# Optimization experiments

Measured on AMD Instinct MI355X. Metric: run time of the kernel, lower is better.

The kernel has to match this reference:

```python
import jax, jax.numpy as jnp
import numpy as np

N_LEVELS = 16
N_FEATS = 2
TABLE_SIZE = 1 << 19          # log2_hashmap_size = 19
BASE_RES = 32
PER_LEVEL_SCALE = 1.3819
RES = 512
CLAMP = 25.133
PRIME_Y = np.uint32(2654435761)
N_PTS = 1 << 19


def hashgrid_encode(table, uv):
    """Instant-NGP style multires hashgrid. table: [L, T, F], uv: [N, 2] in [0,1].
    Returns [N, L*F]."""
    L, T, F = table.shape
    levels = jnp.arange(L)
    res = jnp.floor(BASE_RES * (PER_LEVEL_SCALE ** levels.astype(jnp.float32))).astype(jnp.int32)  # [L]
    # 4 bilinear corner offsets
    offs = jnp.array([[0, 0], [1, 0], [0, 1], [1, 1]], dtype=jnp.int32)  # [4, 2]

    def level_fn(tab_l, res_l):
        pos = uv * res_l.astype(uv.dtype)                       # [N, 2]
        p0 = jnp.clip(jnp.floor(pos).astype(jnp.int32), 0, res_l - 1)
        frac = pos - p0.astype(uv.dtype)                        # [N, 2]
        corners = p0[:, None, :] + offs[None, :, :]             # [N, 4, 2]
        cx = corners[..., 0].astype(jnp.uint32)
        cy = corners[..., 1].astype(jnp.uint32)
        stride = (res_l + 1).astype(jnp.uint32)
        dense_idx = cx + cy * stride                            # dense grid index
        hash_idx = (cx ^ (cy * PRIME_Y)) & jnp.uint32(T - 1)    # spatial hash (T is pow2)
        use_dense = (res_l + 1).astype(jnp.int64) * (res_l + 1).astype(jnp.int64) <= T
        idx = jnp.where(use_dense, dense_idx, hash_idx).astype(jnp.int32)  # [N, 4]
        feats = tab_l[idx]                                      # [N, 4, F] gather
        wx, wy = frac[:, 0], frac[:, 1]
        w = jnp.stack([(1 - wx) * (1 - wy), wx * (1 - wy),
                       (1 - wx) * wy, wx * wy], axis=-1)        # [N, 4]
        return jnp.einsum('ncf,nc->nf', feats, w)               # [N, F]

    out = jax.vmap(level_fn)(table, res)                        # [L, N, F]
    return out.transpose(1, 0, 2).reshape(uv.shape[0], L * F)


def sin_layer(x, W, b):
    h = jnp.clip(x @ W.T + b, -CLAMP, CLAMP)
    return jnp.sin(h)


def setup_inputs() -> dict:
    key = jax.random.key(0)
    ks = jax.random.split(key, 8)
    y = jax.random.randint(ks[0], (N_PTS,), 0, RES, dtype=jnp.int32)
    x = jax.random.randint(ks[1], (N_PTS,), 0, RES, dtype=jnp.int32)
    cam_feat = jax.random.normal(ks[2], (32,), dtype=jnp.float32)
    # NGP tables initialized uniform in [-1e-4, 1e-4]
    table = jax.random.uniform(ks[3], (N_LEVELS, TABLE_SIZE, N_FEATS),
                               minval=-1e-4, maxval=1e-4, dtype=jnp.float32)
    def siren_w(k, outp, inp):
        return jax.random.uniform(k, (outp, inp), minval=-1.0 / inp, maxval=1.0 / inp,
                                  dtype=jnp.float32)
    W1 = siren_w(ks[4], 512, 64)
    W2 = siren_w(ks[5], 512, 512)
    W3 = siren_w(ks[6], 384, 512)
    return {"y": y, "x": x, "cam_feat": cam_feat, "table": table,
            "W1": W1, "b1": jnp.zeros((512,), jnp.float32),
            "W2": W2, "b2": jnp.zeros((512,), jnp.float32),
            "W3": W3, "b3": jnp.zeros((384,), jnp.float32)}


def reference(y, x, cam_feat, table, W1, b1, W2, b2, W3, b3):
    denom = jnp.float32(RES - 1)
    uv = jnp.stack([jnp.clip(x.astype(jnp.float32), 0, RES - 1) / denom,
                    jnp.clip(y.astype(jnp.float32), 0, RES - 1) / denom], axis=-1)  # [N, 2]
    codes = hashgrid_encode(table, uv)                          # [N, 32]
    cam = jnp.broadcast_to(cam_feat[None, :], (codes.shape[0], cam_feat.shape[0]))
    h = jnp.concatenate([codes, cam], axis=-1)                  # [N, 64]
    h = sin_layer(h, W1, b1)
    h = sin_layer(h, W2, b2)
    return sin_layer(h, W3, b3)                                 # [N, 384]
```

## Files before the change

### kernel.cpp

```cpp
#include <hip/hip_runtime.h>

typedef _Float16 half8 __attribute__((ext_vector_type(8)));
typedef _Float16 half4 __attribute__((ext_vector_type(4)));
typedef _Float16 half2v __attribute__((ext_vector_type(2)));
typedef float f32x4 __attribute__((ext_vector_type(4)));

#define TSIZE (1 << 19)
#define TMASK (TSIZE - 1)

__constant__ int c_res[16] = {32, 44, 61, 84, 116, 161, 222, 307,
                              425, 588, 812, 1123, 1551, 2144, 2963, 4095};

__global__ void hg_cvt_all(const float* __restrict__ W1, const float* __restrict__ W2,
                           const float* __restrict__ W3, _Float16* __restrict__ d) {
  int g = blockIdx.x * blockDim.x + threadIdx.x;
  int i = g * 4;
  const float* s;
  if (i < 32768) s = W1 + i;
  else if (i < 32768 + 262144) s = W2 + (i - 32768);
  else s = W3 + (i - 32768 - 262144);
  float4 v = *(const float4*)s;
  half4 h = {(_Float16)v.x, (_Float16)v.y, (_Float16)v.z, (_Float16)v.w};
  *(half4*)(d + i) = h;
}

__device__ __forceinline__ float sin_act(float x) {
  if (__builtin_expect(fabsf(x) > 1.0f, 0))
    return sinf(fminf(fmaxf(x, -25.133f), 25.133f));
  float x2 = x * x;
  float p = 2.75573192e-6f;
  p = fmaf(p, x2, -1.98412698e-4f);
  p = fmaf(p, x2, 8.33333333e-3f);
  p = fmaf(p, x2, -1.66666667e-1f);
  return fmaf(p * x2, x, x);
}

#define XROW 144
#define SBASE 9216
#define SROW 1040
#define LD_X(m, k) (*(const half8*)(&smem[(m) * XROW + (k) * 2]))
#define LD_S(m, k) (*(const half8*)(&smem[SBASE + (m) * SROW + (k) * 2]))
#define ST_S8(m, n, v) \
  do { *(half4*)(&smem[SBASE + (m) * SROW + (n) * 2]) = (v); } while (0)

#define MFMA16 __builtin_amdgcn_mfma_f32_16x16x32_f16

__global__ void __launch_bounds__(512, 4)
hg_fused(const int* __restrict__ ybuf, const int* __restrict__ xbuf,
         const float* __restrict__ cam, const float* __restrict__ table,
         const _Float16* __restrict__ W1h, const float* __restrict__ b1,
         const _Float16* __restrict__ W2h, const float* __restrict__ b2,
         const _Float16* __restrict__ W3h, const float* __restrict__ b3,
         float* __restrict__ out) {
  __shared__ __align__(16) unsigned char smem[75776];
  const int t = threadIdx.x;
  const int lane = t & 63;
  const int wid = t >> 6;
  const int l15 = lane & 15;
  const int lhi = lane >> 4;
  const int pbase = blockIdx.x << 6;
  const f32x4 vzero = {0.f, 0.f, 0.f, 0.f};

  {
    const int sub = t & 15;
    const int res = c_res[sub];
    const float rf = (float)res;
    const unsigned strd = (unsigned)(res + 1);
    const bool dense = (res <= 723);
    const float* tb = table + ((size_t)sub * TSIZE) * 2;
    const float2 cf = ((const float2*)cam)[sub];
    const half2v hc = {(_Float16)cf.x, (_Float16)cf.y};
#pragma unroll
    for (int hh = 0; hh < 2; ++hh) {
      const int m = (t >> 4) + hh * 32;
      const int p = pbase + m;
      const float u = (float)xbuf[p] / 511.0f;
      const float v = (float)ybuf[p] / 511.0f;
      const float px = u * rf, py = v * rf;
      int p0x = (int)floorf(px); p0x = p0x < 0 ? 0 : (p0x > res - 1 ? res - 1 : p0x);
      int p0y = (int)floorf(py); p0y = p0y < 0 ? 0 : (p0y > res - 1 ? res - 1 : p0y);
      const float fx = px - (float)p0x, fy = py - (float)p0y;
      const float w00 = (1.f - fx) * (1.f - fy), w10 = fx * (1.f - fy);
      const float w01 = (1.f - fx) * fy, w11 = fx * fy;
      float c0 = 0.f, c1 = 0.f;
#pragma unroll
      for (int c = 0; c < 4; ++c) {
        const unsigned cx = (unsigned)(p0x + (c & 1));
        const unsigned cy = (unsigned)(p0y + (c >> 1));
        const unsigned idx = dense ? (cx + cy * strd)
                                   : ((cx ^ (cy * 2654435761u)) & TMASK);
        const float2 f = *(const float2*)(tb + (size_t)idx * 2);
        const float w = (c == 0) ? w00 : (c == 1) ? w10 : (c == 2) ? w01 : w11;
        c0 = fmaf(w, f.x, c0);
        c1 = fmaf(w, f.y, c1);
      }
      half2v hf = {(_Float16)c0, (_Float16)c1};
      *(half2v*)(&smem[m * XROW + 4 * sub]) = hf;
      *(half2v*)(&smem[m * XROW + 64 + 4 * sub]) = hc;
    }
  }
  __syncthreads();

  {
    const int n0 = wid << 6;
    f32x4 acc[4][4];
#pragma unroll
    for (int i = 0; i < 4; ++i)
#pragma unroll
      for (int j = 0; j < 4; ++j) acc[i][j] = vzero;
#pragma unroll
    for (int ks = 0; ks < 2; ++ks) {
      const int kk = ks * 32 + lhi * 8;
      half8 bw[4];
#pragma unroll
      for (int nf = 0; nf < 4; ++nf)
        bw[nf] = *(const half8*)(W1h + (n0 + nf * 16 + l15) * 64 + kk);
      half8 ax[4];
#pragma unroll
      for (int mf = 0; mf < 4; ++mf) ax[mf] = LD_X(mf * 16 + l15, kk);
#pragma unroll
      for (int mf = 0; mf < 4; ++mf)
#pragma unroll
        for (int nf = 0; nf < 4; ++nf)
          acc[mf][nf] = MFMA16(bw[nf], ax[mf], acc[mf][nf], 0, 0, 0);
    }
#pragma unroll
    for (int nf = 0; nf < 4; ++nf) {
      const int nb = n0 + nf * 16 + lhi * 4;
      const f32x4 bb = *(const f32x4*)(b1 + nb);
#pragma unroll
      for (int mf = 0; mf < 4; ++mf) {
        half4 pk;
#pragma unroll
        for (int r = 0; r < 4; ++r) pk[r] = (_Float16)sin_act(acc[mf][nf][r] + bb[r]);
        ST_S8(mf * 16 + l15, nb, pk);
      }
    }
  }
  __syncthreads();

  {
    const int n0 = wid << 6;
    f32x4 acc[4][4];
#pragma unroll
    for (int i = 0; i < 4; ++i)
#pragma unroll
      for (int j = 0; j < 4; ++j) acc[i][j] = vzero;
#pragma unroll 4
    for (int ks = 0; ks < 16; ++ks) {
      const int kk = ks * 32 + lhi * 8;
      half8 bw[4];
#pragma unroll
      for (int nf = 0; nf < 4; ++nf)
        bw[nf] = *(const half8*)(W2h + (n0 + nf * 16 + l15) * 512 + kk);
      half8 ax[4];
#pragma unroll
      for (int mf = 0; mf < 4; ++mf) ax[mf] = LD_S(mf * 16 + l15, kk);
#pragma unroll
      for (int mf = 0; mf < 4; ++mf)
#pragma unroll
        for (int nf = 0; nf < 4; ++nf)
          acc[mf][nf] = MFMA16(bw[nf], ax[mf], acc[mf][nf], 0, 0, 0);
    }
    half4 pk[4][4];
#pragma unroll
    for (int nf = 0; nf < 4; ++nf) {
      const f32x4 bb = *(const f32x4*)(b2 + (n0 + nf * 16 + lhi * 4));
#pragma unroll
      for (int mf = 0; mf < 4; ++mf)
#pragma unroll
        for (int r = 0; r < 4; ++r)
          pk[nf][mf][r] = (_Float16)sin_act(acc[mf][nf][r] + bb[r]);
    }
    __syncthreads();
#pragma unroll
    for (int nf = 0; nf < 4; ++nf) {
      const int nb = n0 + nf * 16 + lhi * 4;
#pragma unroll
      for (int mf = 0; mf < 4; ++mf) ST_S8(mf * 16 + l15, nb, pk[nf][mf]);
    }
  }
  __syncthreads();

  {
    const int n0 = wid * 48;
    f32x4 acc[4][3];
#pragma unroll
    for (int i = 0; i < 4; ++i)
#pragma unroll
      for (int j = 0; j < 3; ++j) acc[i][j] = vzero;
#pragma unroll 4
    for (int ks = 0; ks < 16; ++ks) {
      const int kk = ks * 32 + lhi * 8;
      half8 bw[3];
#pragma unroll
      for (int nf = 0; nf < 3; ++nf)
        bw[nf] = *(const half8*)(W3h + (n0 + nf * 16 + l15) * 512 + kk);
      half8 ax[4];
#pragma unroll
      for (int mf = 0; mf < 4; ++mf) ax[mf] = LD_S(mf * 16 + l15, kk);
#pragma unroll
      for (int mf = 0; mf < 4; ++mf)
#pragma unroll
        for (int nf = 0; nf < 3; ++nf)
          acc[mf][nf] = MFMA16(bw[nf], ax[mf], acc[mf][nf], 0, 0, 0);
    }
#pragma unroll
    for (int nf = 0; nf < 3; ++nf) {
      const int nb = n0 + nf * 16 + lhi * 4;
      const f32x4 bb = *(const f32x4*)(b3 + nb);
#pragma unroll
      for (int mf = 0; mf < 4; ++mf) {
        float4 o;
        float* op = &o.x;
#pragma unroll
        for (int r = 0; r < 4; ++r) op[r] = sin_act(acc[mf][nf][r] + bb[r]);
        *(float4*)(out + (size_t)(pbase + mf * 16 + l15) * 384 + nb) = o;
      }
    }
  }
}

extern "C" void kernel_launch(void* const* d_in, const int* in_sizes, int n_in,
                              void* d_out, int out_size, void* d_ws, size_t ws_size,
                              hipStream_t stream) {
  const int* y = (const int*)d_in[0];
  const int* x = (const int*)d_in[1];
  const float* cam = (const float*)d_in[2];
  const float* table = (const float*)d_in[3];
  const float* W1 = (const float*)d_in[4];
  const float* b1 = (const float*)d_in[5];
  const float* W2 = (const float*)d_in[6];
  const float* b2 = (const float*)d_in[7];
  const float* W3 = (const float*)d_in[8];
  const float* b3 = (const float*)d_in[9];
  float* out = (float*)d_out;

  _Float16* Wh = (_Float16*)d_ws;
  _Float16* W1h = Wh;
  _Float16* W2h = W1h + 512 * 64;
  _Float16* W3h = W2h + 512 * 512;

  hg_cvt_all<<<480, 256, 0, stream>>>(W1, W2, W3, Wh);

  const int nblocks = (1 << 19) / 64;
  hg_fused<<<nblocks, 512, 0, stream>>>(y, x, cam, table, W1h, b1, W2h, b2, W3h, b3, out);
}
```

Before: 1.194 ms.

## Double block tile to 128 points, prefetch weights, use fast sine in hidden layers

Each block now covers 128 points with 1024 threads. Pairs of waves split the rows and share the same weight columns, which improves weight reuse through cache, and shared memory is doubled to hold the larger tile. The weight fragments for the next k-step are register-prefetched in the layer-2 and layer-3 loops. The first two sine activations use the hardware __sinf on clamped inputs. The cost is a single block per CU because of the LDS size, more register pressure from launch_bounds(1024,4) and the prefetch buffers, and lower accuracy in the hidden activations.

Result: slower. 1.322 ms (+10.7%).

```diff
diff --git a/kernel.cpp b/kernel.cpp
--- a/kernel.cpp
+++ b/kernel.cpp
@@ -24,7 +24,7 @@
   *(half4*)(d + i) = h;
 }
 
-__device__ __forceinline__ float sin_act(float x) {
+__device__ __forceinline__ float sin_act_precise(float x) {
   if (__builtin_expect(fabsf(x) > 1.0f, 0))
     return sinf(fminf(fmaxf(x, -25.133f), 25.133f));
   float x2 = x * x;
@@ -35,8 +35,12 @@
   return fmaf(p * x2, x, x);
 }
 
+__device__ __forceinline__ float sin_act_fast(float x) {
+  return __sinf(fminf(fmaxf(x, -25.133f), 25.133f));
+}
+
 #define XROW 144
-#define SBASE 9216
+#define SBASE 18432
 #define SROW 1040
 #define LD_X(m, k) (*(const half8*)(&smem[(m) * XROW + (k) * 2]))
 #define LD_S(m, k) (*(const half8*)(&smem[SBASE + (m) * SROW + (k) * 2]))
@@ -45,20 +49,23 @@
 
 #define MFMA16 __builtin_amdgcn_mfma_f32_16x16x32_f16
 
-__global__ void __launch_bounds__(512, 4)
+__global__ void __launch_bounds__(1024, 4)
 hg_fused(const int* __restrict__ ybuf, const int* __restrict__ xbuf,
          const float* __restrict__ cam, const float* __restrict__ table,
          const _Float16* __restrict__ W1h, const float* __restrict__ b1,
          const _Float16* __restrict__ W2h, const float* __restrict__ b2,
          const _Float16* __restrict__ W3h, const float* __restrict__ b3,
          float* __restrict__ out) {
-  __shared__ __align__(16) unsigned char smem[75776];
+  __shared__ __align__(16) unsigned char smem[151552];
   const int t = threadIdx.x;
   const int lane = t & 63;
   const int wid = t >> 6;
   const int l15 = lane & 15;
   const int lhi = lane >> 4;
-  const int pbase = blockIdx.x << 6;
+  const int rowh = wid & 1;
+  const int colg = wid >> 1;
+  const int mrow0 = rowh * 64;
+  const int pbase = blockIdx.x << 7;
   const f32x4 vzero = {0.f, 0.f, 0.f, 0.f};
 
   {
@@ -72,7 +79,7 @@
     const half2v hc = {(_Float16)cf.x, (_Float16)cf.y};
 #pragma unroll
     for (int hh = 0; hh < 2; ++hh) {
-      const int m = (t >> 4) + hh * 32;
+      const int m = (t >> 4) + hh * 64;
       const int p = pbase + m;
       const float u = (float)xbuf[p] / 511.0f;
       const float v = (float)ybuf[p] / 511.0f;
@@ -102,7 +109,7 @@
   __syncthreads();
 
   {
-    const int n0 = wid << 6;
+    const int n0 = colg << 6;
     f32x4 acc[4][4];
 #pragma unroll
     for (int i = 0; i < 4; ++i)
@@ -117,7 +124,7 @@
         bw[nf] = *(const half8*)(W1h + (n0 + nf * 16 + l15) * 64 + kk);
       half8 ax[4];
 #pragma unroll
-      for (int mf = 0; mf < 4; ++mf) ax[mf] = LD_X(mf * 16 + l15, kk);
+      for (int mf = 0; mf < 4; ++mf) ax[mf] = LD_X(mrow0 + mf * 16 + l15, kk);
 #pragma unroll
       for (int mf = 0; mf < 4; ++mf)
 #pragma unroll
@@ -132,78 +139,90 @@
       for (int mf = 0; mf < 4; ++mf) {
         half4 pk;
 #pragma unroll
-        for (int r = 0; r < 4; ++r) pk[r] = (_Float16)sin_act(acc[mf][nf][r] + bb[r]);
-        ST_S8(mf * 16 + l15, nb, pk);
+        for (int r = 0; r < 4; ++r)
+          pk[r] = (_Float16)sin_act_fast(acc[mf][nf][r] + bb[r]);
+        ST_S8(mrow0 + mf * 16 + l15, nb, pk);
       }
     }
   }
   __syncthreads();
 
   {
-    const int n0 = wid << 6;
+    const int n0 = colg << 6;
     f32x4 acc[4][4];
 #pragma unroll
     for (int i = 0; i < 4; ++i)
 #pragma unroll
       for (int j = 0; j < 4; ++j) acc[i][j] = vzero;
-#pragma unroll 4
+    half8 bw[4];
+#pragma unroll
+    for (int nf = 0; nf < 4; ++nf)
+      bw[nf] = *(const half8*)(W2h + (n0 + nf * 16 + l15) * 512 + lhi * 8);
+#pragma unroll 2
     for (int ks = 0; ks < 16; ++ks) {
+      const int kkn = ((ks + 1) & 15) * 32 + lhi * 8;
+      half8 nbw[4];
+#pragma unroll
+      for (int nf = 0; nf < 4; ++nf)
+        nbw[nf] = *(const half8*)(W2h + (n0 + nf * 16 + l15) * 512 + kkn);
       const int kk = ks * 32 + lhi * 8;
-      half8 bw[4];
-#pragma unroll
-      for (int nf = 0; nf < 4; ++nf)
-        bw[nf] = *(const half8*)(W2h + (n0 + nf * 16 + l15) * 512 + kk);
       half8 ax[4];
 #pragma unroll
-      for (int mf = 0; mf < 4; ++mf) ax[mf] = LD_S(mf * 16 + l15, kk);
+      for (int mf = 0; mf < 4; ++mf) ax[mf] = LD_S(mrow0 + mf * 16 + l15, kk);
 #pragma unroll
       for (int mf = 0; mf < 4; ++mf)
 #pragma unroll
         for (int nf = 0; nf < 4; ++nf)
           acc[mf][nf] = MFMA16(bw[nf], ax[mf], acc[mf][nf], 0, 0, 0);
-    }
-    half4 pk[4][4];
-#pragma unroll
-    for (int nf = 0; nf < 4; ++nf) {
-      const f32x4 bb = *(const f32x4*)(b2 + (n0 + nf * 16 + lhi * 4));
-#pragma unroll
-      for (int mf = 0; mf < 4; ++mf)
-#pragma unroll
-        for (int r = 0; r < 4; ++r)
-          pk[nf][mf][r] = (_Float16)sin_act(acc[mf][nf][r] + bb[r]);
+#pragma unroll
+      for (int nf = 0; nf < 4; ++nf) bw[nf] = nbw[nf];
     }
     __syncthreads();
 #pragma unroll
     for (int nf = 0; nf < 4; ++nf) {
       const int nb = n0 + nf * 16 + lhi * 4;
-#pragma unroll
-      for (int mf = 0; mf < 4; ++mf) ST_S8(mf * 16 + l15, nb, pk[nf][mf]);
+      const f32x4 bb = *(const f32x4*)(b2 + nb);
+#pragma unroll
+      for (int mf = 0; mf < 4; ++mf) {
+        half4 pk;
+#pragma unroll
+        for (int r = 0; r < 4; ++r)
+          pk[r] = (_Float16)sin_act_fast(acc[mf][nf][r] + bb[r]);
+        ST_S8(mrow0 + mf * 16 + l15, nb, pk);
+      }
     }
   }
   __syncthreads();
 
   {
-    const int n0 = wid * 48;
+    const int n0 = colg * 48;
     f32x4 acc[4][3];
 #pragma unroll
     for (int i = 0; i < 4; ++i)
 #pragma unroll
       for (int j = 0; j < 3; ++j) acc[i][j] = vzero;
-#pragma unroll 4
+    half8 bw[3];
+#pragma unroll
+    for (int nf = 0; nf < 3; ++nf)
+      bw[nf] = *(const half8*)(W3h + (n0 + nf * 16 + l15) * 512 + lhi * 8);
+#pragma unroll 2
     for (int ks = 0; ks < 16; ++ks) {
+      const int kkn = ((ks + 1) & 15) * 32 + lhi * 8;
+      half8 nbw[3];
+#pragma unroll
+      for (int nf = 0; nf < 3; ++nf)
+        nbw[nf] = *(const half8*)(W3h + (n0 + nf * 16 + l15) * 512 + kkn);
       const int kk = ks * 32 + lhi * 8;
-      half8 bw[3];
-#pragma unroll
-      for (int nf = 0; nf < 3; ++nf)
-        bw[nf] = *(const half8*)(W3h + (n0 + nf * 16 + l15) * 512 + kk);
       half8 ax[4];
 #pragma unroll
-      for (int mf = 0; mf < 4; ++mf) ax[mf] = LD_S(mf * 16 + l15, kk);
+      for (int mf = 0; mf < 4; ++mf) ax[mf] = LD_S(mrow0 + mf * 16 + l15, kk);
 #pragma unroll
       for (int mf = 0; mf < 4; ++mf)
 #pragma unroll
         for (int nf = 0; nf < 3; ++nf)
           acc[mf][nf] = MFMA16(bw[nf], ax[mf], acc[mf][nf], 0, 0, 0);
+#pragma unroll
+      for (int nf = 0; nf < 3; ++nf) bw[nf] = nbw[nf];
     }
 #pragma unroll
     for (int nf = 0; nf < 3; ++nf) {
@@ -214,8 +233,9 @@
         float4 o;
         float* op = &o.x;
 #pragma unroll
-        for (int r = 0; r < 4; ++r) op[r] = sin_act(acc[mf][nf][r] + bb[r]);
-        *(float4*)(out + (size_t)(pbase + mf * 16 + l15) * 384 + nb) = o;
+        for (int r = 0; r < 4; ++r)
+          op[r] = sin_act_precise(acc[mf][nf][r] + bb[r]);
+        *(float4*)(out + (size_t)(pbase + mrow0 + mf * 16 + l15) * 384 + nb) = o;
       }
     }
   }
@@ -243,6 +263,6 @@
 
   hg_cvt_all<<<480, 256, 0, stream>>>(W1, W2, W3, Wh);
 
-  const int nblocks = (1 << 19) / 64;
-  hg_fused<<<nblocks, 512, 0, stream>>>(y, x, cam, table, W1h, b1, W2h, b2, W3h, b3, out);
-}
+  const int nblocks = (1 << 19) / 128;
+  hg_fused<<<nblocks, 1024, 0, stream>>>(y, x, cam, table, W1h, b1, W2h, b2, W3h, b3, out);
+}
```
